# Kernel optimization log

Measured on AMD Instinct MI355X. Metric: run time of the kernel, lower is better.

## Reference

```python
import jax, jax.numpy as jnp
import numpy as np
import math

NUM_SLOTS = 512
DIM = 1024

def _l2norm(x, eps=1e-12):
    # matches F.normalize(p=2, dim=-1): x / max(||x||, eps)
    n = jnp.linalg.norm(x, axis=-1, keepdims=True)
    return x / jnp.maximum(n, eps)

def setup_inputs() -> dict:
    key = jax.random.key(0)
    ks = jax.random.split(key, 10)
    d = DIM
    s = 1.0 / math.sqrt(d)
    inp = {
        "mamba_states": jax.random.normal(ks[0], (8, 4096, d), dtype=jnp.float32),
        "memory": jax.random.normal(ks[1], (NUM_SLOTS, d), dtype=jnp.float32),  # stand-in for orthogonal init
        "Wq": jax.random.uniform(ks[2], (d, d), jnp.float32, -s, s),
        "bq": jax.random.uniform(ks[3], (d,), jnp.float32, -s, s),
        "Wk": jax.random.uniform(ks[4], (d, d), jnp.float32, -s, s),
        "bk": jax.random.uniform(ks[5], (d,), jnp.float32, -s, s),
        "Wv": jax.random.uniform(ks[6], (d, d), jnp.float32, -s, s),
        "bv": jax.random.uniform(ks[7], (d,), jnp.float32, -s, s),
        "Wg": jax.random.uniform(ks[8], (2 * d, d), jnp.float32, -1.0 / math.sqrt(2 * d), 1.0 / math.sqrt(2 * d)),
        "bg": jax.random.uniform(ks[9], (d,), jnp.float32, -1.0 / math.sqrt(2 * d), 1.0 / math.sqrt(2 * d)),
    }
    return inp

def reference(mamba_states, memory, Wq, bq, Wk, bk, Wv, bv, Wg, bg):
    d = mamba_states.shape[-1]
    Q = mamba_states @ Wq + bq                      # [b, s, d]
    K = memory @ Wk + bk                            # [n, d]
    V = memory @ Wv + bv                            # [n, d]
    Qn = _l2norm(Q)
    Kn = _l2norm(K)
    scores = jnp.einsum('bsd,nd->bsn', Qn, Kn) / jnp.sqrt(jnp.float32(d))
    w = jax.nn.softmax(scores, axis=-1)             # [b, s, n]
    R = jnp.einsum('bsn,nd->bsd', w, V)             # [b, s, d]
    gate_in = jnp.concatenate([mamba_states, R], axis=-1)  # [b, s, 2d]
    g = jax.nn.sigmoid(gate_in @ Wg + bg)           # [b, s, d]
    return g * mamba_states + (1.0 - g) * R
```

## Files before the change

### kernel.cpp

```cpp
#include <hip/hip_runtime.h>
#include <cstdint>

typedef __attribute__((ext_vector_type(8))) __bf16 bf16x8;
typedef __attribute__((ext_vector_type(4))) float f32x4;

__device__ __forceinline__ unsigned short f2bf(float f) {
  unsigned u = __float_as_uint(f);
  unsigned r = (u + 0x7FFFu + ((u >> 16) & 1u)) >> 16;
  return (unsigned short)r;
}
__device__ __forceinline__ float bf2f(unsigned short u) {
  return __uint_as_float(((unsigned)u) << 16);
}

__device__ __forceinline__ __attribute__((address_space(3))) void* to_lds(void* p) {
  return (__attribute__((address_space(3))) void*)p;
}
__device__ __forceinline__ const __attribute__((address_space(1))) void* to_glb(const void* p) {
  return (const __attribute__((address_space(1))) void*)p;
}

__global__ void k_transpose_bf16(const float* __restrict__ in, unsigned short* __restrict__ out,
                                 int R, int C) {
  __shared__ float tile[32][33];
  int c0 = blockIdx.x * 32, r0 = blockIdx.y * 32;
  int tx = threadIdx.x, ty = threadIdx.y;
  #pragma unroll
  for (int i = 0; i < 32; i += 8)
    tile[ty + i][tx] = in[(size_t)(r0 + ty + i) * C + c0 + tx];
  __syncthreads();
  #pragma unroll
  for (int i = 0; i < 32; i += 8)
    out[(size_t)(c0 + ty + i) * R + r0 + tx] = f2bf(tile[tx][ty + i]);
}

__global__ void k_convert_bf16(const float4* __restrict__ in, ushort4* __restrict__ out, int n4) {
  int i = blockIdx.x * blockDim.x + threadIdx.x;
  if (i < n4) {
    float4 v = in[i];
    ushort4 o; o.x = f2bf(v.x); o.y = f2bf(v.y); o.z = f2bf(v.z); o.w = f2bf(v.w);
    out[i] = o;
  }
}

__global__ void k_stage_x(const float4* __restrict__ X, unsigned short* __restrict__ gate_in, int n4) {
  int i = blockIdx.x * blockDim.x + threadIdx.x;
  if (i < n4) {
    int flat = i << 2;
    int row = flat >> 10, col = flat & 1023;
    float4 v = X[i];
    ushort4 o; o.x = f2bf(v.x); o.y = f2bf(v.y); o.z = f2bf(v.z); o.w = f2bf(v.w);
    *(ushort4*)(gate_in + (size_t)row * 2048 + col) = o;
  }
}

__global__ void k_concat_bias(const float* __restrict__ bk, const float* __restrict__ bv,
                              float* __restrict__ bkv) {
  int i = blockIdx.x * blockDim.x + threadIdx.x;
  if (i < 2048) bkv[i] = (i < 1024) ? bk[i] : bv[i - 1024];
}

__global__ void k_post_kv(const float4* __restrict__ KV, unsigned short* __restrict__ Kn,
                          unsigned short* __restrict__ Vt) {
  int row = blockIdx.x;
  int tid = threadIdx.x;
  const float4* r = KV + (size_t)row * 512;
  float4 k4 = r[tid];
  float4 v4 = r[256 + tid];
  float s = k4.x * k4.x + k4.y * k4.y + k4.z * k4.z + k4.w * k4.w;
  #pragma unroll
  for (int m = 32; m; m >>= 1) s += __shfl_xor(s, m, 64);
  __shared__ float red[4];
  if ((tid & 63) == 0) red[tid >> 6] = s;
  __syncthreads();
  float tot = red[0] + red[1] + red[2] + red[3];
  float inv = 1.0f / fmaxf(sqrtf(tot), 1e-12f);
  ushort4 o; o.x = f2bf(k4.x * inv); o.y = f2bf(k4.y * inv);
  o.z = f2bf(k4.z * inv); o.w = f2bf(k4.w * inv);
  *(ushort4*)(Kn + (size_t)row * 1024 + tid * 4) = o;
  int vc = tid * 4;
  Vt[(size_t)(vc + 0) * 512 + row] = f2bf(v4.x);
  Vt[(size_t)(vc + 1) * 512 + row] = f2bf(v4.y);
  Vt[(size_t)(vc + 2) * 512 + row] = f2bf(v4.z);
  Vt[(size_t)(vc + 3) * 512 + row] = f2bf(v4.w);
}

__global__ void k_softmax(const float4* __restrict__ S, const float* __restrict__ norm2,
                          unsigned short* __restrict__ W) {
  int tid = threadIdx.x;
  int wv = tid >> 6, lane = tid & 63;
  int row = blockIdx.x * 4 + wv;
  float alpha = 0.03125f * rsqrtf(fmaxf(norm2[row], 1e-24f));
  const float4* sr = S + (size_t)row * 128;
  float4 a = sr[lane], b = sr[64 + lane];
  a.x *= alpha; a.y *= alpha; a.z *= alpha; a.w *= alpha;
  b.x *= alpha; b.y *= alpha; b.z *= alpha; b.w *= alpha;
  float m = fmaxf(fmaxf(fmaxf(a.x, a.y), fmaxf(a.z, a.w)),
                  fmaxf(fmaxf(b.x, b.y), fmaxf(b.z, b.w)));
  #pragma unroll
  for (int o = 32; o; o >>= 1) m = fmaxf(m, __shfl_xor(m, o, 64));
  a.x = __expf(a.x - m); a.y = __expf(a.y - m); a.z = __expf(a.z - m); a.w = __expf(a.w - m);
  b.x = __expf(b.x - m); b.y = __expf(b.y - m); b.z = __expf(b.z - m); b.w = __expf(b.w - m);
  float s = a.x + a.y + a.z + a.w + b.x + b.y + b.z + b.w;
  #pragma unroll
  for (int o = 32; o; o >>= 1) s += __shfl_xor(s, o, 64);
  float inv = 1.0f / s;
  ushort4 oa, ob;
  oa.x = f2bf(a.x * inv); oa.y = f2bf(a.y * inv); oa.z = f2bf(a.z * inv); oa.w = f2bf(a.w * inv);
  ob.x = f2bf(b.x * inv); ob.y = f2bf(b.y * inv); ob.z = f2bf(b.z * inv); ob.w = f2bf(b.w * inv);
  ushort4* wr = (ushort4*)(W + (size_t)row * 512);
  wr[lane] = oa; wr[64 + lane] = ob;
}

template <int MODE>
__global__ __launch_bounds__(256, 2) void k_gemm(
    const unsigned short* __restrict__ A, int lda,
    const unsigned short* __restrict__ B, int ldb,
    const float* __restrict__ bias, float scale,
    float* __restrict__ C, int ldc,
    unsigned short* __restrict__ Cb, int ldcb,
    float* __restrict__ Cnorm,
    int K) {
  __shared__ __align__(16) unsigned short As[128 * 64];
  __shared__ __align__(16) unsigned short Bs[128 * 64];
  const int tid = threadIdx.x;
  const int lane = tid & 63, w = tid >> 6;

  int mt, nt;
  {
    int f = blockIdx.y * gridDim.x + blockIdx.x;
    int NTg = gridDim.x, MTg = gridDim.y;
    if ((MTg & 7) == 0) {
      int xcd = f & 7;
      int j = f >> 3;
      nt = j % NTg;
      mt = (j / NTg) * 8 + xcd;
    } else {
      mt = blockIdx.y; nt = blockIdx.x;
    }
  }
  const int m0 = mt * 128, n0 = nt * 128;

  const int srow = lane >> 3;
  const int schunk = (lane & 7) ^ srow;
  const unsigned short* gA = A + (size_t)(m0 + w * 8 + srow) * lda + schunk * 8;
  const unsigned short* gB = B + (size_t)(n0 + w * 8 + srow) * ldb + schunk * 8;
  unsigned short* lA = As + (w * 8) * 64;
  unsigned short* lB = Bs + (w * 8) * 64;

  f32x4 acc[4][4];
  f32x4 zero = {0.f, 0.f, 0.f, 0.f};
  #pragma unroll
  for (int i = 0; i < 4; ++i)
    #pragma unroll
    for (int j = 0; j < 4; ++j) acc[i][j] = zero;

  const int fr = lane & 15, q = lane >> 4;
  const int wr = (w >> 1) * 64, wc = (w & 1) * 64;

  for (int k0 = 0; k0 < K; k0 += 64) {
    #pragma unroll
    for (int i = 0; i < 4; ++i) {
      __builtin_amdgcn_global_load_lds(to_glb(gA + (size_t)i * 32 * lda + k0),
                                       to_lds(lA + i * 32 * 64), 16, 0, 0);
      __builtin_amdgcn_global_load_lds(to_glb(gB + (size_t)i * 32 * ldb + k0),
                                       to_lds(lB + i * 32 * 64), 16, 0, 0);
    }
    __syncthreads();
    #pragma unroll
    for (int ks = 0; ks < 2; ++ks) {
      bf16x8 af[4], bfr[4];
      const int p = (ks * 4 + q) ^ (lane & 7);
      #pragma unroll
      for (int mi = 0; mi < 4; ++mi) {
        af[mi] = *(const bf16x8*)(As + (wr + mi * 16 + fr) * 64 + p * 8);
        bfr[mi] = *(const bf16x8*)(Bs + (wc + mi * 16 + fr) * 64 + p * 8);
      }
      #pragma unroll
      for (int mi = 0; mi < 4; ++mi)
        #pragma unroll
        for (int ni = 0; ni < 4; ++ni)
          acc[mi][ni] = __builtin_amdgcn_mfma_f32_16x16x32_bf16(af[mi], bfr[ni], acc[mi][ni], 0, 0, 0);
    }
    __syncthreads();
  }

  if (MODE == 1) {
    #pragma unroll
    for (int mi = 0; mi < 4; ++mi) {
      float s2[4] = {0.f, 0.f, 0.f, 0.f};
      #pragma unroll
      for (int ni = 0; ni < 4; ++ni) {
        const int gc = n0 + wc + ni * 16 + fr;
        const float bv = bias[gc];
        #pragma unroll
        for (int r = 0; r < 4; ++r) {
          const int gr = m0 + wr + mi * 16 + q * 4 + r;
          float c = acc[mi][ni][r] + bv;
          Cb[(size_t)gr * ldcb + gc] = f2bf(c);
          s2[r] += c * c;
        }
      }
      #pragma unroll
      for (int r = 0; r < 4; ++r) {
        float v = s2[r];
        v += __shfl_xor(v, 1, 64);
        v += __shfl_xor(v, 2, 64);
        v += __shfl_xor(v, 4, 64);
        v += __shfl_xor(v, 8, 64);
        if (fr == 0) atomicAdd(Cnorm + (m0 + wr + mi * 16 + q * 4 + r), v);
      }
    }
  } else {
    #pragma unroll
    for (int ni = 0; ni < 4; ++ni) {
      const int gc = n0 + wc + ni * 16 + fr;
      const float bv = bias ? bias[gc] : 0.0f;
      #pragma unroll
      for (int mi = 0; mi < 4; ++mi) {
        #pragma unroll
        for (int r = 0; r < 4; ++r) {
          const int gr = m0 + wr + mi * 16 + q * 4 + r;
          float c = acc[mi][ni][r] * scale + bv;
          if (MODE == 0) {
            C[(size_t)gr * ldc + gc] = c;
          } else if (MODE == 2) {
            Cb[(size_t)gr * ldcb + gc] = f2bf(c);
          } else {
            float g = 1.0f / (1.0f + __expf(-c));
            float x = bf2f(Cb[(size_t)gr * ldcb + gc]);
            float rr = bf2f(Cb[(size_t)gr * ldcb + 1024 + gc]);
            C[(size_t)gr * ldc + gc] = g * x + (1.0f - g) * rr;
          }
        }
      }
    }
  }
}

extern "C" void kernel_launch(void* const* d_in, const int* in_sizes, int n_in,
                              void* d_out, int out_size, void* d_ws, size_t ws_size,
                              hipStream_t stream) {
  const float* X   = (const float*)d_in[0];
  const float* mem = (const float*)d_in[1];
  const float* Wq  = (const float*)d_in[2];
  const float* bq  = (const float*)d_in[3];
  const float* Wk  = (const float*)d_in[4];
  const float* bk  = (const float*)d_in[5];
  const float* Wv  = (const float*)d_in[6];
  const float* bv  = (const float*)d_in[7];
  const float* Wg  = (const float*)d_in[8];
  const float* bg  = (const float*)d_in[9];
  float* out = (float*)d_out;

  const int T = 32768, D = 1024, NS = 512;

  char* p = (char*)d_ws;
  auto alloc = [&](size_t b) { char* r = p; p += (b + 255) & ~(size_t)255; return r; };
  unsigned short* WqT    = (unsigned short*)alloc((size_t)D * D * 2);
  unsigned short* WkvT   = (unsigned short*)alloc((size_t)2 * D * D * 2);
  unsigned short* WgT    = (unsigned short*)alloc((size_t)D * 2 * D * 2);
  unsigned short* memb   = (unsigned short*)alloc((size_t)NS * D * 2);
  float*          bkv    = (float*)alloc((size_t)2 * D * 4);
  float*          KV     = (float*)alloc((size_t)NS * 2 * D * 4);
  unsigned short* Kn     = (unsigned short*)alloc((size_t)NS * D * 2);
  unsigned short* Vt     = (unsigned short*)alloc((size_t)D * NS * 2);
  unsigned short* gatein = (unsigned short*)alloc((size_t)T * 2 * D * 2);
  unsigned short* Qb     = (unsigned short*)alloc((size_t)T * D * 2);
  unsigned short* Wsm    = (unsigned short*)alloc((size_t)T * NS * 2);
  float*          S      = (float*)alloc((size_t)T * NS * 4);
  float*          norm2  = (float*)alloc((size_t)T * 4);

  hipMemsetAsync(norm2, 0, (size_t)T * 4, stream);

  k_transpose_bf16<<<dim3(32, 32), dim3(32, 8), 0, stream>>>(Wq, WqT, D, D);
  k_transpose_bf16<<<dim3(32, 32), dim3(32, 8), 0, stream>>>(Wk, WkvT, D, D);
  k_transpose_bf16<<<dim3(32, 32), dim3(32, 8), 0, stream>>>(Wv, WkvT + (size_t)D * D, D, D);
  k_transpose_bf16<<<dim3(32, 64), dim3(32, 8), 0, stream>>>(Wg, WgT, 2 * D, D);
  k_convert_bf16<<<512, 256, 0, stream>>>((const float4*)mem, (ushort4*)memb, NS * D / 4);
  k_concat_bias<<<8, 256, 0, stream>>>(bk, bv, bkv);
  k_stage_x<<<T * D / 4 / 256, 256, 0, stream>>>((const float4*)X, gatein, T * D / 4);

  k_gemm<0><<<dim3(2 * D / 128, NS / 128), 256, 0, stream>>>(
      memb, D, WkvT, D, bkv, 1.0f, KV, 2 * D, nullptr, 0, nullptr, D);
  k_post_kv<<<NS, 256, 0, stream>>>((const float4*)KV, Kn, Vt);

  k_gemm<1><<<dim3(D / 128, T / 128), 256, 0, stream>>>(
      gatein, 2 * D, WqT, D, bq, 1.0f, nullptr, 0, Qb, D, norm2, D);

  k_gemm<0><<<dim3(NS / 128, T / 128), 256, 0, stream>>>(
      Qb, D, Kn, D, nullptr, 1.0f, S, NS, nullptr, 0, nullptr, D);
  k_softmax<<<T / 4, 256, 0, stream>>>((const float4*)S, norm2, Wsm);

  k_gemm<2><<<dim3(D / 128, T / 128), 256, 0, stream>>>(
      Wsm, NS, Vt, NS, nullptr, 1.0f, nullptr, 0, gatein + D, 2 * D, nullptr, NS);

  k_gemm<3><<<dim3(D / 128, T / 128), 256, 0, stream>>>(
      gatein, 2 * D, WgT, 2 * D, bg, 1.0f, out, D, gatein, 2 * D, nullptr, 2 * D);

  (void)in_sizes; (void)n_in; (void)out_size; (void)ws_size;
}
```

Measured before the change: 636.5 us.

## Reassociate gate GEMM through attention weights and fuse Q with gate-X projection

Splits the gate projection into an X part and an R part. The X part is computed alongside Q in a single wide GEMM (Wq and Wg_top concatenated), and the R part is reassociated as W·(V·Wg_bottom), using a precomputed 512x1024 matrix. This turns the K=2048 gate GEMM into a K=512 GEMM over the softmax weights. Scores are also stored in bf16 instead of fp32 to halve softmax traffic. The cost is extra intermediate buffers (Lb, Rb) and extra bf16 rounding of the scores and of the gate logits, which may change accuracy.

Result: slower. 652.4 us (+2.5%).

```diff
diff --git a/kernel.cpp b/kernel.cpp
--- a/kernel.cpp
+++ b/kernel.cpp
@@ -3,6 +3,7 @@
 
 typedef __attribute__((ext_vector_type(8))) __bf16 bf16x8;
 typedef __attribute__((ext_vector_type(4))) float f32x4;
+typedef __attribute__((ext_vector_type(8))) unsigned short u16x8;
 
 __device__ __forceinline__ unsigned short f2bf(float f) {
   unsigned u = __float_as_uint(f);
@@ -43,25 +44,14 @@
   }
 }
 
-__global__ void k_stage_x(const float4* __restrict__ X, unsigned short* __restrict__ gate_in, int n4) {
+__global__ void k_concat_bias(const float* __restrict__ b0, const float* __restrict__ b1,
+                              float* __restrict__ bc) {
   int i = blockIdx.x * blockDim.x + threadIdx.x;
-  if (i < n4) {
-    int flat = i << 2;
-    int row = flat >> 10, col = flat & 1023;
-    float4 v = X[i];
-    ushort4 o; o.x = f2bf(v.x); o.y = f2bf(v.y); o.z = f2bf(v.z); o.w = f2bf(v.w);
-    *(ushort4*)(gate_in + (size_t)row * 2048 + col) = o;
-  }
-}
-
-__global__ void k_concat_bias(const float* __restrict__ bk, const float* __restrict__ bv,
-                              float* __restrict__ bkv) {
-  int i = blockIdx.x * blockDim.x + threadIdx.x;
-  if (i < 2048) bkv[i] = (i < 1024) ? bk[i] : bv[i - 1024];
+  if (i < 2048) bc[i] = (i < 1024) ? b0[i] : b1[i - 1024];
 }
 
 __global__ void k_post_kv(const float4* __restrict__ KV, unsigned short* __restrict__ Kn,
-                          unsigned short* __restrict__ Vt) {
+                          unsigned short* __restrict__ Vt, unsigned short* __restrict__ Vb) {
   int row = blockIdx.x;
   int tid = threadIdx.x;
   const float4* r = KV + (size_t)row * 512;
@@ -78,38 +68,40 @@
   ushort4 o; o.x = f2bf(k4.x * inv); o.y = f2bf(k4.y * inv);
   o.z = f2bf(k4.z * inv); o.w = f2bf(k4.w * inv);
   *(ushort4*)(Kn + (size_t)row * 1024 + tid * 4) = o;
+  ushort4 ov; ov.x = f2bf(v4.x); ov.y = f2bf(v4.y); ov.z = f2bf(v4.z); ov.w = f2bf(v4.w);
+  *(ushort4*)(Vb + (size_t)row * 1024 + tid * 4) = ov;
   int vc = tid * 4;
-  Vt[(size_t)(vc + 0) * 512 + row] = f2bf(v4.x);
-  Vt[(size_t)(vc + 1) * 512 + row] = f2bf(v4.y);
-  Vt[(size_t)(vc + 2) * 512 + row] = f2bf(v4.z);
-  Vt[(size_t)(vc + 3) * 512 + row] = f2bf(v4.w);
-}
-
-__global__ void k_softmax(const float4* __restrict__ S, const float* __restrict__ norm2,
+  Vt[(size_t)(vc + 0) * 512 + row] = ov.x;
+  Vt[(size_t)(vc + 1) * 512 + row] = ov.y;
+  Vt[(size_t)(vc + 2) * 512 + row] = ov.z;
+  Vt[(size_t)(vc + 3) * 512 + row] = ov.w;
+}
+
+__global__ void k_softmax(const unsigned short* __restrict__ S, const float* __restrict__ norm2,
                           unsigned short* __restrict__ W) {
   int tid = threadIdx.x;
   int wv = tid >> 6, lane = tid & 63;
   int row = blockIdx.x * 4 + wv;
   float alpha = 0.03125f * rsqrtf(fmaxf(norm2[row], 1e-24f));
-  const float4* sr = S + (size_t)row * 128;
-  float4 a = sr[lane], b = sr[64 + lane];
-  a.x *= alpha; a.y *= alpha; a.z *= alpha; a.w *= alpha;
-  b.x *= alpha; b.y *= alpha; b.z *= alpha; b.w *= alpha;
-  float m = fmaxf(fmaxf(fmaxf(a.x, a.y), fmaxf(a.z, a.w)),
-                  fmaxf(fmaxf(b.x, b.y), fmaxf(b.z, b.w)));
+  u16x8 u = *(const u16x8*)(S + (size_t)row * 512 + lane * 8);
+  float v[8];
+  #pragma unroll
+  for (int i = 0; i < 8; ++i) v[i] = bf2f(u[i]) * alpha;
+  float m = v[0];
+  #pragma unroll
+  for (int i = 1; i < 8; ++i) m = fmaxf(m, v[i]);
   #pragma unroll
   for (int o = 32; o; o >>= 1) m = fmaxf(m, __shfl_xor(m, o, 64));
-  a.x = __expf(a.x - m); a.y = __expf(a.y - m); a.z = __expf(a.z - m); a.w = __expf(a.w - m);
-  b.x = __expf(b.x - m); b.y = __expf(b.y - m); b.z = __expf(b.z - m); b.w = __expf(b.w - m);
-  float s = a.x + a.y + a.z + a.w + b.x + b.y + b.z + b.w;
+  float s = 0.f;
+  #pragma unroll
+  for (int i = 0; i < 8; ++i) { v[i] = __expf(v[i] - m); s += v[i]; }
   #pragma unroll
   for (int o = 32; o; o >>= 1) s += __shfl_xor(s, o, 64);
   float inv = 1.0f / s;
-  ushort4 oa, ob;
-  oa.x = f2bf(a.x * inv); oa.y = f2bf(a.y * inv); oa.z = f2bf(a.z * inv); oa.w = f2bf(a.w * inv);
-  ob.x = f2bf(b.x * inv); ob.y = f2bf(b.y * inv); ob.z = f2bf(b.z * inv); ob.w = f2bf(b.w * inv);
-  ushort4* wr = (ushort4*)(W + (size_t)row * 512);
-  wr[lane] = oa; wr[64 + lane] = ob;
+  u16x8 ou;
+  #pragma unroll
+  for (int i = 0; i < 8; ++i) ou[i] = f2bf(v[i] * inv);
+  *(u16x8*)(W + (size_t)row * 512 + lane * 8) = ou;
 }
 
 template <int MODE>
@@ -119,6 +111,10 @@
     const float* __restrict__ bias, float scale,
     float* __restrict__ C, int ldc,
     unsigned short* __restrict__ Cb, int ldcb,
+    unsigned short* __restrict__ Cb2,
+    const unsigned short* __restrict__ auxL,
+    const unsigned short* __restrict__ auxX,
+    const unsigned short* __restrict__ auxR,
     float* __restrict__ Cnorm,
     int K) {
   __shared__ __align__(16) unsigned short As[128 * 64];
@@ -185,7 +181,7 @@
     __syncthreads();
   }
 
-  if (MODE == 1) {
+  if (MODE == 5 && n0 < 1024) {
     #pragma unroll
     for (int mi = 0; mi < 4; ++mi) {
       float s2[4] = {0.f, 0.f, 0.f, 0.f};
@@ -215,22 +211,27 @@
     #pragma unroll
     for (int ni = 0; ni < 4; ++ni) {
       const int gc = n0 + wc + ni * 16 + fr;
-      const float bv = bias ? bias[gc] : 0.0f;
+      const float bv = (MODE == 4 || MODE == 6) ? 0.0f : (bias ? bias[gc] : 0.0f);
       #pragma unroll
       for (int mi = 0; mi < 4; ++mi) {
         #pragma unroll
         for (int r = 0; r < 4; ++r) {
           const int gr = m0 + wr + mi * 16 + q * 4 + r;
-          float c = acc[mi][ni][r] * scale + bv;
           if (MODE == 0) {
-            C[(size_t)gr * ldc + gc] = c;
+            C[(size_t)gr * ldc + gc] = acc[mi][ni][r] * scale + bv;
           } else if (MODE == 2) {
-            Cb[(size_t)gr * ldcb + gc] = f2bf(c);
+            Cb[(size_t)gr * ldcb + gc] = f2bf(acc[mi][ni][r] * scale + bv);
+          } else if (MODE == 4) {
+            Cb[(size_t)gc * ldcb + gr] = f2bf(acc[mi][ni][r]);
+          } else if (MODE == 5) {
+            Cb2[(size_t)gr * 1024 + (gc - 1024)] = f2bf(acc[mi][ni][r] + bv);
           } else {
-            float g = 1.0f / (1.0f + __expf(-c));
-            float x = bf2f(Cb[(size_t)gr * ldcb + gc]);
-            float rr = bf2f(Cb[(size_t)gr * ldcb + 1024 + gc]);
-            C[(size_t)gr * ldc + gc] = g * x + (1.0f - g) * rr;
+            const size_t idx = (size_t)gr * 1024 + gc;
+            float l = bf2f(auxL[idx]);
+            float g = 1.0f / (1.0f + __expf(-(acc[mi][ni][r] + l)));
+            float x = bf2f(auxX[idx]);
+            float rr = bf2f(auxR[idx]);
+            C[idx] = g * x + (1.0f - g) * rr;
           }
         }
       }
@@ -257,46 +258,56 @@
 
   char* p = (char*)d_ws;
   auto alloc = [&](size_t b) { char* r = p; p += (b + 255) & ~(size_t)255; return r; };
-  unsigned short* WqT    = (unsigned short*)alloc((size_t)D * D * 2);
-  unsigned short* WkvT   = (unsigned short*)alloc((size_t)2 * D * D * 2);
-  unsigned short* WgT    = (unsigned short*)alloc((size_t)D * 2 * D * 2);
-  unsigned short* memb   = (unsigned short*)alloc((size_t)NS * D * 2);
-  float*          bkv    = (float*)alloc((size_t)2 * D * 4);
-  float*          KV     = (float*)alloc((size_t)NS * 2 * D * 4);
-  unsigned short* Kn     = (unsigned short*)alloc((size_t)NS * D * 2);
-  unsigned short* Vt     = (unsigned short*)alloc((size_t)D * NS * 2);
-  unsigned short* gatein = (unsigned short*)alloc((size_t)T * 2 * D * 2);
-  unsigned short* Qb     = (unsigned short*)alloc((size_t)T * D * 2);
-  unsigned short* Wsm    = (unsigned short*)alloc((size_t)T * NS * 2);
-  float*          S      = (float*)alloc((size_t)T * NS * 4);
-  float*          norm2  = (float*)alloc((size_t)T * 4);
+  unsigned short* WB    = (unsigned short*)alloc((size_t)2 * D * D * 2);
+  unsigned short* WkvT  = (unsigned short*)alloc((size_t)2 * D * D * 2);
+  unsigned short* WgrT  = (unsigned short*)alloc((size_t)D * D * 2);
+  unsigned short* memb  = (unsigned short*)alloc((size_t)NS * D * 2);
+  float*          bkv   = (float*)alloc((size_t)2 * D * 4);
+  float*          bqg   = (float*)alloc((size_t)2 * D * 4);
+  float*          KV    = (float*)alloc((size_t)NS * 2 * D * 4);
+  unsigned short* Kn    = (unsigned short*)alloc((size_t)NS * D * 2);
+  unsigned short* Vt    = (unsigned short*)alloc((size_t)D * NS * 2);
+  unsigned short* Vb    = (unsigned short*)alloc((size_t)NS * D * 2);
+  unsigned short* VgT   = (unsigned short*)alloc((size_t)D * NS * 2);
+  unsigned short* Xb    = (unsigned short*)alloc((size_t)T * D * 2);
+  unsigned short* Qb    = (unsigned short*)alloc((size_t)T * D * 2);
+  unsigned short* Lb    = (unsigned short*)alloc((size_t)T * D * 2);
+  unsigned short* Sb    = (unsigned short*)alloc((size_t)T * NS * 2);
+  unsigned short* Wsm   = (unsigned short*)alloc((size_t)T * NS * 2);
+  unsigned short* Rb    = (unsigned short*)alloc((size_t)T * D * 2);
+  float*          norm2 = (float*)alloc((size_t)T * 4);
 
   hipMemsetAsync(norm2, 0, (size_t)T * 4, stream);
 
-  k_transpose_bf16<<<dim3(32, 32), dim3(32, 8), 0, stream>>>(Wq, WqT, D, D);
+  k_transpose_bf16<<<dim3(32, 32), dim3(32, 8), 0, stream>>>(Wq, WB, D, D);
+  k_transpose_bf16<<<dim3(32, 32), dim3(32, 8), 0, stream>>>(Wg, WB + (size_t)D * D, D, D);
+  k_transpose_bf16<<<dim3(32, 32), dim3(32, 8), 0, stream>>>(Wg + (size_t)D * D, WgrT, D, D);
   k_transpose_bf16<<<dim3(32, 32), dim3(32, 8), 0, stream>>>(Wk, WkvT, D, D);
   k_transpose_bf16<<<dim3(32, 32), dim3(32, 8), 0, stream>>>(Wv, WkvT + (size_t)D * D, D, D);
-  k_transpose_bf16<<<dim3(32, 64), dim3(32, 8), 0, stream>>>(Wg, WgT, 2 * D, D);
   k_convert_bf16<<<512, 256, 0, stream>>>((const float4*)mem, (ushort4*)memb, NS * D / 4);
   k_concat_bias<<<8, 256, 0, stream>>>(bk, bv, bkv);
-  k_stage_x<<<T * D / 4 / 256, 256, 0, stream>>>((const float4*)X, gatein, T * D / 4);
-
-  k_gemm<0><<<dim3(2 * D / 128, NS / 128), 256, 0, stream>>>(
-      memb, D, WkvT, D, bkv, 1.0f, KV, 2 * D, nullptr, 0, nullptr, D);
-  k_post_kv<<<NS, 256, 0, stream>>>((const float4*)KV, Kn, Vt);
-
-  k_gemm<1><<<dim3(D / 128, T / 128), 256, 0, stream>>>(
-      gatein, 2 * D, WqT, D, bq, 1.0f, nullptr, 0, Qb, D, norm2, D);
-
-  k_gemm<0><<<dim3(NS / 128, T / 128), 256, 0, stream>>>(
-      Qb, D, Kn, D, nullptr, 1.0f, S, NS, nullptr, 0, nullptr, D);
-  k_softmax<<<T / 4, 256, 0, stream>>>((const float4*)S, norm2, Wsm);
-
-  k_gemm<2><<<dim3(D / 128, T / 128), 256, 0, stream>>>(
-      Wsm, NS, Vt, NS, nullptr, 1.0f, nullptr, 0, gatein + D, 2 * D, nullptr, NS);
-
-  k_gemm<3><<<dim3(D / 128, T / 128), 256, 0, stream>>>(
-      gatein, 2 * D, WgT, 2 * D, bg, 1.0f, out, D, gatein, 2 * D, nullptr, 2 * D);
+  k_concat_bias<<<8, 256, 0, stream>>>(bq, bg, bqg);
+  k_convert_bf16<<<T * D / 4 / 256, 256, 0, stream>>>((const float4*)X, (ushort4*)Xb, T * D / 4);
+
+  k_gemm<0><<<dim3(16, 4), 256, 0, stream>>>(
+      memb, D, WkvT, D, bkv, 1.0f, KV, 2 * D, nullptr, 0, nullptr, nullptr, nullptr, nullptr, nullptr, D);
+  k_post_kv<<<NS, 256, 0, stream>>>((const float4*)KV, Kn, Vt, Vb);
+
+  k_gemm<4><<<dim3(8, 4), 256, 0, stream>>>(
+      Vb, D, WgrT, D, nullptr, 1.0f, nullptr, 0, VgT, NS, nullptr, nullptr, nullptr, nullptr, nullptr, D);
+
+  k_gemm<5><<<dim3(16, 256), 256, 0, stream>>>(
+      Xb, D, WB, D, bqg, 1.0f, nullptr, 0, Qb, D, Lb, nullptr, nullptr, nullptr, norm2, D);
+
+  k_gemm<2><<<dim3(4, 256), 256, 0, stream>>>(
+      Qb, D, Kn, D, nullptr, 1.0f, nullptr, 0, Sb, NS, nullptr, nullptr, nullptr, nullptr, nullptr, D);
+  k_softmax<<<T / 4, 256, 0, stream>>>(Sb, norm2, Wsm);
+
+  k_gemm<2><<<dim3(8, 256), 256, 0, stream>>>(
+      Wsm, NS, Vt, NS, nullptr, 1.0f, nullptr, 0, Rb, D, nullptr, nullptr, nullptr, nullptr, nullptr, NS);
+
+  k_gemm<6><<<dim3(8, 256), 256, 0, stream>>>(
+      Wsm, NS, VgT, NS, nullptr, 1.0f, out, D, nullptr, 0, nullptr, Lb, Xb, Rb, nullptr, NS);
 
   (void)in_sizes; (void)n_in; (void)out_size; (void)ws_size;
 }
```
